# Kernel tuning notes

Measured on AMD Instinct MI355X. Metric: run time of the kernel, lower is better.

## Reference

```python
import jax, jax.numpy as jnp
import numpy as np

N, E, B = 10000, 160000, 256
IN, DESC = 57, 1217
# (in_dim, heads, out_per_head) for the 4 GATConv layers
CONV_DIMS = [(57, 5, 114), (570, 5, 171), (855, 5, 114), (570, 1, 570)]
FC_DIMS = [(1024 + DESC, 1024), (1024, 2048), (2048, 1024), (1024, 256), (256, 1)]


def setup_inputs() -> dict:
    key = jax.random.key(0)
    cnt = [0]
    def p(shape, scale=0.05):
        cnt[0] += 1
        return jax.random.normal(jax.random.fold_in(key, cnt[0]), shape, jnp.float32) * scale
    d = {}
    d["x"] = jax.random.normal(jax.random.fold_in(key, 100), (N, IN), jnp.float32)
    d["edge_index"] = jax.random.randint(jax.random.fold_in(key, 101), (2, E), 0, N)
    d["batch"] = jnp.sort(jax.random.randint(jax.random.fold_in(key, 102), (N,), 0, B))
    d["desc"] = jax.random.normal(jax.random.fold_in(key, 103), (B, DESC), jnp.float32)
    for i, (ci, H, C) in enumerate(CONV_DIMS, 1):
        d[f"W{i}"] = p((ci, H * C))
        d[f"as{i}"] = p((H, C))
        d[f"ad{i}"] = p((H, C))
        d[f"b{i}"] = jnp.zeros((H * C,), jnp.float32)
    d["Wg"] = p((570, 1024)); d["bg"] = jnp.zeros((1024,), jnp.float32)
    for i, (ci, co) in enumerate(FC_DIMS, 1):
        d[f"Wf{i}"] = p((ci, co))
        d[f"bf{i}"] = jnp.zeros((co,), jnp.float32)
    return d


def gat_conv(x, src, dst, W, a_src, a_dst, b):
    """PyG GATConv (eval mode: attention dropout off), self-loops already in src/dst."""
    n = x.shape[0]
    H, C = a_src.shape
    h = (x @ W).reshape(n, H, C)                      # [N,H,C]
    al_s = (h * a_src).sum(-1)                         # [N,H]
    al_d = (h * a_dst).sum(-1)                         # [N,H]
    e = jax.nn.leaky_relu(al_s[src] + al_d[dst], 0.2)  # [E,H]
    # segment softmax over destination node
    m = jax.ops.segment_max(e, dst, num_segments=n)
    e = jnp.exp(e - m[dst])
    s = jax.ops.segment_sum(e, dst, num_segments=n)
    alpha = e / (s[dst] + 1e-16)                       # [E,H]
    msg = h[src] * alpha[:, :, None]                   # [E,H,C]
    out = jax.ops.segment_sum(msg, dst, num_segments=n)
    return out.reshape(n, H * C) + b


def reference(x, edge_index, batch, desc,
              W1, as1, ad1, b1, W2, as2, ad2, b2,
              W3, as3, ad3, b3, W4, as4, ad4, b4,
              Wg, bg, Wf1, bf1, Wf2, bf2, Wf3, bf3, Wf4, bf4, Wf5, bf5):
    n = x.shape[0]
    loops = jnp.arange(n)
    src = jnp.concatenate([edge_index[0], loops])
    dst = jnp.concatenate([edge_index[1], loops])
    h = x
    for W, a_s, a_d, b in [(W1, as1, ad1, b1), (W2, as2, ad2, b2),
                           (W3, as3, ad3, b3), (W4, as4, ad4, b4)]:
        h = jax.nn.relu(gat_conv(h, src, dst, W, a_s, a_d, b))
    pooled = jax.ops.segment_sum(h, batch, num_segments=B)   # global_add_pool [B,570]
    g = pooled @ Wg + bg
    z = jnp.concatenate([g, desc], axis=1)                    # [B, 2241]
    z = jax.nn.relu(z @ Wf1 + bf1)
    z = jax.nn.relu(z @ Wf2 + bf2)
    z = jax.nn.relu(z @ Wf3 + bf3)
    z = jax.nn.relu(z @ Wf4 + bf4)
    return z @ Wf5 + bf5                                      # [B,1]
```

## Files before the change

kernel.cpp:

```cpp
#include <hip/hip_runtime.h>
#include <hip/hip_bf16.h>
#include <math.h>

#define NNODES 10000
#define NEDGES 160000
#define NB     256
#define ETOT   (NEDGES + NNODES)
#define INDIM  57
#define DESCD  1217

static inline size_t align256(size_t x) { return (x + 255) & ~size_t(255); }

typedef _Float16 half8_t __attribute__((ext_vector_type(8)));
typedef _Float16 half4v_t __attribute__((ext_vector_type(4)));
typedef _Float16 half2_t __attribute__((ext_vector_type(2)));
typedef float f32x4 __attribute__((ext_vector_type(4)));

__device__ inline void gload_lds16(const void* g, void* l) {
  __builtin_amdgcn_global_load_lds((const __attribute__((address_space(1))) void*)g,
                                   (__attribute__((address_space(3))) void*)l, 16, 0, 0);
}

__device__ inline float wave_sum(float v) {
#pragma unroll
  for (int o = 32; o > 0; o >>= 1) v += __shfl_xor(v, o);
  return v;
}

__global__ void count_kernel(const int* __restrict__ ei, int* __restrict__ deg) {
  int e = blockIdx.x * blockDim.x + threadIdx.x;
  if (e < ETOT) {
    int dst = (e < NEDGES) ? ei[NEDGES + e] : (e - NEDGES);
    atomicAdd(&deg[dst], 1);
  }
}

__global__ __launch_bounds__(1024) void scan_kernel(const int* __restrict__ deg,
                                                    int* __restrict__ row_ptr,
                                                    int* __restrict__ cursor) {
  __shared__ int part[1024];
  const int CHUNK = (NNODES + 1023) / 1024;
  int t = threadIdx.x;
  int start = t * CHUNK;
  int sum = 0;
  for (int i = 0; i < CHUNK; ++i) {
    int idx = start + i;
    if (idx < NNODES) sum += deg[idx];
  }
  part[t] = sum;
  __syncthreads();
  for (int off = 1; off < 1024; off <<= 1) {
    int v = (t >= off) ? part[t - off] : 0;
    __syncthreads();
    part[t] += v;
    __syncthreads();
  }
  int run = (t > 0) ? part[t - 1] : 0;
  for (int i = 0; i < CHUNK; ++i) {
    int idx = start + i;
    if (idx < NNODES) {
      row_ptr[idx] = run;
      cursor[idx] = run;
      run += deg[idx];
    }
  }
  if (t == 1023) row_ptr[NNODES] = ETOT;
}

__global__ void scatter_kernel(const int* __restrict__ ei, int* __restrict__ cursor,
                               int* __restrict__ csr_src) {
  int e = blockIdx.x * blockDim.x + threadIdx.x;
  if (e < ETOT) {
    int src, dst;
    if (e < NEDGES) { src = ei[e]; dst = ei[NEDGES + e]; }
    else            { src = e - NEDGES; dst = src; }
    int idx = atomicAdd(&cursor[dst], 1);
    csr_src[idx] = src;
  }
}

__global__ void convert_x_kernel(const float* __restrict__ x, _Float16* __restrict__ x16) {
  int t = blockIdx.x * blockDim.x + threadIdx.x;
  if (t >= NNODES * 64) return;
  int n = t >> 6, k = t & 63;
  x16[t] = (_Float16)((k < INDIM) ? x[n * INDIM + k] : 0.f);
}

struct TMat { const float* src; _Float16* dst; int K, N, Kpad, tiles_k, tile_base;
              int Cn, Cnp, Ck, Ckp; };
struct TParams { TMat m[9]; };

__global__ __launch_bounds__(256) void transpose_w_kernel(TParams P, int nm) {
  __shared__ float tile[64][65];
  int bt = blockIdx.x;
  int mi = 0;
#pragma unroll
  for (int i = 1; i < 9; ++i)
    if (i < nm && bt >= P.m[i].tile_base) mi = i;
  TMat m = P.m[mi];
  int lt = bt - m.tile_base;
  int tk = lt % m.tiles_k, tn = lt / m.tiles_k;
  int k0 = tk * 64, n0 = tn * 64;
  int c = threadIdx.x & 63, r4 = threadIdx.x >> 6;
#pragma unroll
  for (int i = 0; i < 16; ++i) {
    int kr = r4 + i * 4;
    int gk = k0 + kr, gn = n0 + c;
    tile[kr][c] = (gk < m.K && gn < m.N) ? m.src[(size_t)gk * m.N + gn] : 0.f;
  }
  __syncthreads();
#pragma unroll
  for (int i = 0; i < 16; ++i) {
    int nr = r4 + i * 4;
    int gn = n0 + nr, gk = k0 + c;
    if (gn < m.N && gk < m.K) {
      int np = gn + (gn / m.Cn) * (m.Cnp - m.Cn);
      int kp = gk + (gk / m.Ck) * (m.Ckp - m.Ck);
      m.dst[(size_t)np * m.Kpad + kp] = (_Float16)tile[c][nr];
    }
  }
}

struct LMat { const float* W; const float* as; const float* ad; _Float16* dst;
              int K, HC, C, H, Kpad, la, wave_base, Ck, Ckp; };

__global__ __launch_bounds__(256) void logitw_kernel(LMat m0, LMat m1, LMat m2, LMat m3,
                                                     int nwaves) {
  int gw = (blockIdx.x * 256 + threadIdx.x) >> 6;
  int lane = threadIdx.x & 63;
  if (gw >= nwaves) return;
  LMat m = m3;
  if (gw < m1.wave_base) m = m0;
  else if (gw < m2.wave_base) m = m1;
  else if (gw < m3.wave_base) m = m2;
  int li = gw - m.wave_base;
  int H2 = 2 * m.H;
  int k = li / H2, r = li - k * H2;
  int h = (r >= m.H) ? r - m.H : r;
  const float* a = (r >= m.H) ? m.ad : m.as;
  float s = 0.f;
  for (int c = lane; c < m.C; c += 64)
    s += m.W[(size_t)k * m.HC + h * m.C + c] * a[h * m.C + c];
  s = wave_sum(s);
  int kp = k + (k / m.Ck) * (m.Ckp - m.Ck);
  if (lane == 0) m.dst[(size_t)(m.la + r) * m.Kpad + kp] = (_Float16)s;
}

__global__ void pooled16_kernel(const float* __restrict__ pooled, _Float16* __restrict__ p16) {
  int t = blockIdx.x * blockDim.x + threadIdx.x;
  if (t >= NB * 576) return;
  int b = t / 576, c = t - b * 576;
  p16[t] = (_Float16)((c < 570) ? pooled[b * 570 + c] : 0.f);
}

__global__ void desc_fill_kernel(const float* __restrict__ desc, _Float16* __restrict__ z16) {
  int t = blockIdx.x * blockDim.x + threadIdx.x;
  if (t >= NB * 1280) return;
  int b = t / 1280, i = t - b * 1280;
  z16[(size_t)b * 2304 + 1024 + i] = (_Float16)((i < DESCD) ? desc[b * DESCD + i] : 0.f);
}

__global__ __launch_bounds__(256) void mfma_gemm_kernel(
    const _Float16* __restrict__ A, const _Float16* __restrict__ Bt,
    _Float16* __restrict__ C, int M, int Kpad, int Nreal, int ldc) {
  __shared__ __align__(16) char smem[32768];
  char* AsB = smem;
  char* BsB = smem + 16384;
  int tid = threadIdx.x;
  int lane = tid & 63, wid = tid >> 6;
  int l15 = lane & 15, g = lane >> 4;
  int wr = wid >> 1, wc = wid & 1;
  int m0 = blockIdx.y * 128, n0 = blockIdx.x * 128;
  f32x4 acc[4][4];
#pragma unroll
  for (int i = 0; i < 4; ++i)
#pragma unroll
    for (int j = 0; j < 4; ++j) acc[i][j] = (f32x4){0.f, 0.f, 0.f, 0.f};

  int KT = Kpad >> 6;
  int ra = tid >> 3;
  int c8 = tid & 7;
  const _Float16* srcA[4];
  const _Float16* srcB[4];
#pragma unroll
  for (int i = 0; i < 4; ++i) {
    int rr = i * 32 + ra;
    int cs = c8 ^ (rr & 7);
    int gaA = min(m0 + rr, M - 1);
    srcA[i] = A + (size_t)gaA * Kpad + cs * 8;
    srcB[i] = Bt + (size_t)(n0 + rr) * Kpad + cs * 8;
  }
  char* ldsA = AsB + wid * 1024;
  char* ldsB = BsB + wid * 1024;

  for (int kt = 0; kt < KT; ++kt) {
    int k0 = kt << 6;
    __syncthreads();
#pragma unroll
    for (int i = 0; i < 4; ++i) {
      gload_lds16(srcA[i] + k0, ldsA + i * 4096);
      gload_lds16(srcB[i] + k0, ldsB + i * 4096);
    }
    __syncthreads();
#pragma unroll
    for (int kk = 0; kk < 2; ++kk) {
      half8_t af[4], bf[4];
#pragma unroll
      for (int f = 0; f < 4; ++f) {
        int raf = wr * 64 + f * 16 + l15;
        af[f] = *(const half8_t*)(AsB + raf * 128 + (((kk * 4 + g) ^ (raf & 7)) << 4));
        int cb = wc * 64 + f * 16 + l15;
        bf[f] = *(const half8_t*)(BsB + cb * 128 + (((kk * 4 + g) ^ (cb & 7)) << 4));
      }
#pragma unroll
      for (int fm = 0; fm < 4; ++fm)
#pragma unroll
        for (int fn = 0; fn < 4; ++fn)
          acc[fm][fn] = __builtin_amdgcn_mfma_f32_16x16x32_f16(af[fm], bf[fn], acc[fm][fn], 0, 0, 0);
    }
  }
#pragma unroll
  for (int fm = 0; fm < 4; ++fm) {
    int gmb = m0 + wr * 64 + fm * 16 + g * 4;
#pragma unroll
    for (int fn = 0; fn < 4; ++fn) {
      int gn = n0 + wc * 64 + fn * 16 + l15;
      if (gn >= Nreal) continue;
#pragma unroll
      for (int j = 0; j < 4; ++j) {
        int gm = gmb + j;
        if (gm < M) C[(size_t)gm * ldc + gn] = (_Float16)acc[fm][fn][j];
      }
    }
  }
}

__global__ __launch_bounds__(256) void mfma_gemm64_kernel(
    const _Float16* __restrict__ A, const _Float16* __restrict__ Bt,
    const float* __restrict__ bias, _Float16* __restrict__ O,
    int Kpad, int ldc, int relu) {
  __shared__ __align__(16) char smem[16384];
  char* AsB = smem;
  char* BsB = smem + 8192;
  int tid = threadIdx.x;
  int lane = tid & 63, wid = tid >> 6;
  int l15 = lane & 15, g = lane >> 4;
  int wr = wid >> 1, wc = wid & 1;
  int m0 = blockIdx.y * 64, n0 = blockIdx.x * 64;
  f32x4 acc[2][2];
#pragma unroll
  for (int i = 0; i < 2; ++i)
#pragma unroll
    for (int j = 0; j < 2; ++j) acc[i][j] = (f32x4){0.f, 0.f, 0.f, 0.f};

  int KT = Kpad >> 6;
  int r = tid >> 2;
  half8_t pa[2], pb[2];
#pragma unroll
  for (int i = 0; i < 2; ++i) {
    int cc = (tid & 3) + 4 * i;
    int cs = cc ^ (r & 7);
    pa[i] = *(const half8_t*)(A + (size_t)(m0 + r) * Kpad + cs * 8);
    pb[i] = *(const half8_t*)(Bt + (size_t)(n0 + r) * Kpad + cs * 8);
  }
  for (int kt = 0; kt < KT; ++kt) {
    __syncthreads();
#pragma unroll
    for (int i = 0; i < 2; ++i) {
      int cc = (tid & 3) + 4 * i;
      *(half8_t*)(AsB + r * 128 + cc * 16) = pa[i];
      *(half8_t*)(BsB + r * 128 + cc * 16) = pb[i];
    }
    __syncthreads();
    if (kt + 1 < KT) {
      int k0 = (kt + 1) << 6;
#pragma unroll
      for (int i = 0; i < 2; ++i) {
        int cc = (tid & 3) + 4 * i;
        int cs = cc ^ (r & 7);
        pa[i] = *(const half8_t*)(A + (size_t)(m0 + r) * Kpad + k0 + cs * 8);
        pb[i] = *(const half8_t*)(Bt + (size_t)(n0 + r) * Kpad + k0 + cs * 8);
      }
    }
#pragma unroll
    for (int kk = 0; kk < 2; ++kk) {
      half8_t af[2], bf[2];
#pragma unroll
      for (int f = 0; f < 2; ++f) {
        int ra = wr * 32 + f * 16 + l15;
        af[f] = *(const half8_t*)(AsB + ra * 128 + (((kk * 4 + g) ^ (ra & 7)) << 4));
        int cb = wc * 32 + f * 16 + l15;
        bf[f] = *(const half8_t*)(BsB + cb * 128 + (((kk * 4 + g) ^ (cb & 7)) << 4));
      }
#pragma unroll
      for (int fm = 0; fm < 2; ++fm)
#pragma unroll
        for (int fn = 0; fn < 2; ++fn)
          acc[fm][fn] = __builtin_amdgcn_mfma_f32_16x16x32_f16(af[fm], bf[fn], acc[fm][fn], 0, 0, 0);
    }
  }
#pragma unroll
  for (int fm = 0; fm < 2; ++fm) {
    int gmb = m0 + wr * 32 + fm * 16 + g * 4;
#pragma unroll
    for (int fn = 0; fn < 2; ++fn) {
      int gn = n0 + wc * 32 + fn * 16 + l15;
      float bv = bias[gn];
#pragma unroll
      for (int j = 0; j < 4; ++j) {
        float v = acc[fm][fn][j] + bv;
        if (relu) v = fmaxf(v, 0.f);
        O[(size_t)(gmb + j) * ldc + gn] = (_Float16)v;
      }
    }
  }
}

__global__ __launch_bounds__(256) void fc5_kernel(const _Float16* __restrict__ A,
                                                  const float* __restrict__ w,
                                                  const float* __restrict__ b,
                                                  float* __restrict__ out) {
  int wid = threadIdx.x >> 6, lane = threadIdx.x & 63;
  int m = blockIdx.x * 4 + wid;
  if (m >= NB) return;
  float s = 0.f;
  for (int k = lane; k < 256; k += 64) s += (float)A[m * 256 + k] * w[k];
  s = wave_sum(s);
  if (lane == 0) out[m] = s + b[0];
}

template <int H>
__global__ __launch_bounds__(256) void att_kernel_t(const _Float16* __restrict__ hbuf,
                                                    int ldh, int la,
                                                    const int* __restrict__ row_ptr,
                                                    const int* __restrict__ csr_src,
                                                    _Float16* __restrict__ alpha_t,
                                                    float* __restrict__ sinv) {
  int wid = threadIdx.x >> 6, lane = threadIdx.x & 63;
  int n = blockIdx.x * 4 + wid;
  if (n >= NNODES) return;
  int rp = row_ptr[n], deg = row_ptr[n + 1] - rp;
  float ad[H], ssum[H];
#pragma unroll
  for (int h = 0; h < H; ++h) {
    ad[h] = (float)hbuf[(size_t)n * ldh + la + H + h];
    ssum[h] = 0.f;
  }
  for (int j = lane; j < deg; j += 64) {
    int s = csr_src[rp + j];
    half8_t v = *(const half8_t*)(hbuf + (size_t)s * ldh + la);
#pragma unroll
    for (int h = 0; h < H; ++h) {
      float e = (float)v[h] + ad[h];
      e = (e >= 0.f) ? e : 0.2f * e;
      e = fminf(e, 10.f);
      float x = expf(e);
      ssum[h] += x;
      alpha_t[(size_t)h * ETOT + rp + j] = (_Float16)x;
    }
  }
#pragma unroll
  for (int h = 0; h < H; ++h) {
    float s = wave_sum(ssum[h]);
    if (lane == 0) sinv[h * NNODES + n] = 1.f / (s + 1e-16f);
  }
}

__global__ __launch_bounds__(256) void agg_kernel(const _Float16* __restrict__ hbuf,
                                                  const _Float16* __restrict__ alpha_t,
                                                  const int* __restrict__ row_ptr,
                                                  const int* __restrict__ csr_src,
                                                  const float* __restrict__ bias,
                                                  const float* __restrict__ sinv,
                                                  _Float16* __restrict__ h16o,
                                                  int C, int Cpad, int ldh, int ldo,
                                                  int HCpad, int nchunks) {
  int wid = threadIdx.x >> 6, lane = threadIdx.x & 63;
  int gw = blockIdx.x * 4 + wid;
  int n = gw / nchunks, chunk = gw - n * nchunks;
  if (n >= NNODES) return;
  int k0 = chunk * 512 + lane * 8;
  if (k0 >= ldo) return;
  _Float16* op = h16o + (size_t)n * ldo + k0;
  if (k0 >= HCpad) { *(half8_t*)op = (half8_t){}; return; }
  int h0 = k0 / Cpad;
  int off = k0 - h0 * Cpad;
  const _Float16* A0 = alpha_t + (size_t)h0 * ETOT;
  const _Float16* hb = hbuf + k0;
  int rp = row_ptr[n], re = row_ptr[n + 1];
  half2_t acc0{}, acc1{}, acc2{}, acc3{};
  auto step = [&](int s, _Float16 a) {
    half8_t v = *(const half8_t*)(hb + (size_t)s * ldh);
    half2_t av{a, a};
    acc0 += av * half2_t{v[0], v[1]};
    acc1 += av * half2_t{v[2], v[3]};
    acc2 += av * half2_t{v[4], v[5]};
    acc3 += av * half2_t{v[6], v[7]};
  };
  int j = rp;
  for (; j < re && (j & 3); ++j) step(csr_src[j], A0[j]);
  for (; j + 8 <= re; j += 8) {
    int4 sa = *(const int4*)(csr_src + j);
    int4 sb = *(const int4*)(csr_src + j + 4);
    half4v_t aa = *(const half4v_t*)(A0 + j);
    half4v_t ab = *(const half4v_t*)(A0 + j + 4);
    step(sa.x, aa[0]); step(sa.y, aa[1]); step(sa.z, aa[2]); step(sa.w, aa[3]);
    step(sb.x, ab[0]); step(sb.y, ab[1]); step(sb.z, ab[2]); step(sb.w, ab[3]);
  }
  for (; j + 4 <= re; j += 4) {
    int4 sa = *(const int4*)(csr_src + j);
    half4v_t aa = *(const half4v_t*)(A0 + j);
    step(sa.x, aa[0]); step(sa.y, aa[1]); step(sa.z, aa[2]); step(sa.w, aa[3]);
  }
  for (; j < re; ++j) step(csr_src[j], A0[j]);
  float sc = sinv[h0 * NNODES + n];
  int base = h0 * C + off;
  int nreal = C - off;
  float af[8] = {(float)acc0[0], (float)acc0[1], (float)acc1[0], (float)acc1[1],
                 (float)acc2[0], (float)acc2[1], (float)acc3[0], (float)acc3[1]};
  half8_t o;
#pragma unroll
  for (int i = 0; i < 8; ++i) {
    float bv = bias[base + ((i < nreal) ? i : 0)];
    o[i] = (i < nreal) ? (_Float16)fmaxf(af[i] * sc + bv, 0.f) : (_Float16)0.f;
  }
  *(half8_t*)op = o;
}

__global__ __launch_bounds__(256) void pool_kernel(const _Float16* __restrict__ h4,
                                                   const int* __restrict__ batch,
                                                   float* __restrict__ pooled, int F, int ldh) {
  int wid = threadIdx.x >> 6, lane = threadIdx.x & 63;
  int n = blockIdx.x * 4 + wid;
  if (n >= NNODES) return;
  int b = batch[n];
  for (int k = lane; k < F; k += 64)
    atomicAdd(&pooled[(size_t)b * F + k], (float)h4[(size_t)n * ldh + k]);
}

extern "C" void kernel_launch(void* const* d_in, const int* in_sizes, int n_in,
                              void* d_out, int out_size, void* d_ws, size_t ws_size,
                              hipStream_t stream) {
  const float* x    = (const float*)d_in[0];
  const int*   ei   = (const int*)d_in[1];
  const int*   batch= (const int*)d_in[2];
  const float* desc = (const float*)d_in[3];
  const float* W1 = (const float*)d_in[4];  const float* as1 = (const float*)d_in[5];
  const float* ad1 = (const float*)d_in[6]; const float* b1 = (const float*)d_in[7];
  const float* W2 = (const float*)d_in[8];  const float* as2 = (const float*)d_in[9];
  const float* ad2 = (const float*)d_in[10];const float* b2 = (const float*)d_in[11];
  const float* W3 = (const float*)d_in[12]; const float* as3 = (const float*)d_in[13];
  const float* ad3 = (const float*)d_in[14];const float* b3 = (const float*)d_in[15];
  const float* W4 = (const float*)d_in[16]; const float* as4 = (const float*)d_in[17];
  const float* ad4 = (const float*)d_in[18];const float* b4 = (const float*)d_in[19];
  const float* Wg = (const float*)d_in[20]; const float* bg = (const float*)d_in[21];
  const float* Wf1 = (const float*)d_in[22];const float* bf1 = (const float*)d_in[23];
  const float* Wf2 = (const float*)d_in[24];const float* bf2 = (const float*)d_in[25];
  const float* Wf3 = (const float*)d_in[26];const float* bf3 = (const float*)d_in[27];
  const float* Wf4 = (const float*)d_in[28];const float* bf4 = (const float*)d_in[29];
  const float* Wf5 = (const float*)d_in[30];const float* bf5 = (const float*)d_in[31];
  float* out = (float*)d_out;

  char* p = (char*)d_ws;
  size_t off = 0;
  auto alloc = [&](size_t bytes) -> char* {
    char* r = p + off;
    off = align256(off + bytes);
    return r;
  };
  int*      deg     = (int*)alloc(sizeof(int) * NNODES);
  int*      row_ptr = (int*)alloc(sizeof(int) * (NNODES + 1));
  int*      cursor  = (int*)alloc(sizeof(int) * NNODES);
  int*      csr_src = (int*)alloc(sizeof(int) * ETOT);
  _Float16* alpha_t = (_Float16*)alloc(sizeof(_Float16) * (size_t)5 * ETOT);
  float*    sinv    = (float*)alloc(sizeof(float) * 5 * NNODES);
  _Float16* x16     = (_Float16*)alloc(sizeof(_Float16) * (size_t)NNODES * 64);
  _Float16* hA16    = (_Float16*)alloc(sizeof(_Float16) * ((size_t)NNODES * 896 + 1024));
  _Float16* h16     = (_Float16*)alloc(sizeof(_Float16) * ((size_t)NNODES * 896 + 1024));
  size_t wt_begin = off;
  _Float16* WtL1 = (_Float16*)alloc(sizeof(_Float16) * 640 * 64);
  _Float16* WtL2 = (_Float16*)alloc(sizeof(_Float16) * 896 * 640);
  _Float16* WtL3 = (_Float16*)alloc(sizeof(_Float16) * 640 * 896);
  _Float16* WtL4 = (_Float16*)alloc(sizeof(_Float16) * 640 * 640);
  _Float16* WtG  = (_Float16*)alloc(sizeof(_Float16) * 1024 * 576);
  _Float16* WtF1 = (_Float16*)alloc(sizeof(_Float16) * 1024 * 2304);
  _Float16* WtF2 = (_Float16*)alloc(sizeof(_Float16) * 2048 * 1024);
  _Float16* WtF3 = (_Float16*)alloc(sizeof(_Float16) * 1024 * 2048);
  _Float16* WtF4 = (_Float16*)alloc(sizeof(_Float16) * 256 * 1024);
  size_t wt_end = off;
  float*    pooled  = (float*)alloc(sizeof(float) * NB * 570);
  _Float16* p16     = (_Float16*)alloc(sizeof(_Float16) * NB * 576);
  _Float16* z16     = (_Float16*)alloc(sizeof(_Float16) * NB * 2304);
  _Float16* t16     = (_Float16*)alloc(sizeof(_Float16) * NB * 2048);
  _Float16* u16     = (_Float16*)alloc(sizeof(_Float16) * NB * 2048);
  _Float16* v16     = (_Float16*)alloc(sizeof(_Float16) * NB * 256);
  (void)ws_size;

  hipMemsetAsync(deg, 0, sizeof(int) * NNODES, stream);
  {
    dim3 g((ETOT + 255) / 256);
    count_kernel<<<g, 256, 0, stream>>>(ei, deg);
    scan_kernel<<<1, 1024, 0, stream>>>(deg, row_ptr, cursor);
    scatter_kernel<<<g, 256, 0, stream>>>(ei, cursor, csr_src);
  }
  convert_x_kernel<<<(NNODES * 64 + 255) / 256, 256, 0, stream>>>(x, x16);

  hipMemsetAsync(p + wt_begin, 0, wt_end - wt_begin, stream);
  {
    auto tiles = [](int K, int N) { return ((K + 63) / 64) * ((N + 63) / 64); };
    TParams tp;
    int base = 0;
    auto add = [&](int i, const float* src, _Float16* dst, int K, int N, int Kpad,
                   int Cn, int Cnp, int Ck, int Ckp) {
      tp.m[i] = { src, dst, K, N, Kpad, (K + 63) / 64, base, Cn, Cnp, Ck, Ckp };
      base += tiles(K, N);
    };
    add(0, W1,  WtL1, INDIM,        570,   64, 114, 120, INDIM, INDIM);
    add(1, W2,  WtL2, 570,          855,  640, 171, 176, 114, 120);
    add(2, W3,  WtL3, 855,          570,  896, 114, 120, 171, 176);
    add(3, W4,  WtL4, 570,          570,  640, 570, 570, 114, 120);
    add(4, Wg,  WtG,  570,          1024,  576, 1024, 1024, 570, 570);
    add(5, Wf1, WtF1, 1024 + DESCD, 1024, 2304, 1024, 1024, 2304, 2304);
    add(6, Wf2, WtF2, 1024,         2048, 1024, 2048, 2048, 1024, 1024);
    add(7, Wf3, WtF3, 2048,         1024, 2048, 1024, 1024, 2048, 2048);
    add(8, Wf4, WtF4, 1024,          256, 1024, 256, 256, 1024, 1024);
    transpose_w_kernel<<<base, 256, 0, stream>>>(tp, 9);
  }
  {
    LMat m0 = { W1, as1, ad1, WtL1, INDIM, 570, 114, 5,  64, 600, 0, INDIM, INDIM };
    LMat m1 = { W2, as2, ad2, WtL2, 570,   855, 171, 5, 640, 880, INDIM * 10, 114, 120 };
    LMat m2 = { W3, as3, ad3, WtL3, 855,   570, 114, 5, 896, 600, INDIM * 10 + 5700, 171, 176 };
    LMat m3 = { W4, as4, ad4, WtL4, 570,   570, 570, 1, 640, 576, INDIM * 10 + 5700 + 8550, 114, 120 };
    int nwaves = INDIM * 10 + 5700 + 8550 + 1140;
    logitw_kernel<<<(nwaves * 64 + 255) / 256, 256, 0, stream>>>(m0, m1, m2, m3, nwaves);
  }

  dim3 gnode((NNODES + 3) / 4);

  struct LayerDef { _Float16* Wt; const float* b;
                    int H, C, Cpad, HCpad, Kpad, Npad, ldh, la, Nreal, ldo; };
  LayerDef L[4] = {
    { WtL1, b1, 5, 114, 120, 600,  64, 640, 616, 600, 610, 640 },
    { WtL2, b2, 5, 171, 176, 880, 640, 896, 896, 880, 890, 896 },
    { WtL3, b3, 5, 114, 120, 600, 896, 640, 616, 600, 610, 640 },
    { WtL4, b4, 1, 570, 576, 576, 640, 640, 584, 576, 578, 576 },
  };
  for (int l = 0; l < 4; ++l) {
    {
      const _Float16* Ain = (l == 0) ? x16 : h16;
      dim3 g(L[l].Npad / 128, (NNODES + 127) / 128);
      mfma_gemm_kernel<<<g, 256, 0, stream>>>(Ain, L[l].Wt, hA16, NNODES, L[l].Kpad,
                                              L[l].Nreal, L[l].ldh);
    }
    if (L[l].H == 5)
      att_kernel_t<5><<<gnode, 256, 0, stream>>>(hA16, L[l].ldh, L[l].la,
                                                 row_ptr, csr_src, alpha_t, sinv);
    else
      att_kernel_t<1><<<gnode, 256, 0, stream>>>(hA16, L[l].ldh, L[l].la,
                                                 row_ptr, csr_src, alpha_t, sinv);
    {
      int nchunks = (L[l].ldo + 511) / 512;
      dim3 g((NNODES * nchunks + 3) / 4);
      agg_kernel<<<g, 256, 0, stream>>>(hA16, alpha_t, row_ptr, csr_src, L[l].b, sinv, h16,
                                        L[l].C, L[l].Cpad, L[l].ldh, L[l].ldo,
                                        L[l].HCpad, nchunks);
    }
  }

  hipMemsetAsync(pooled, 0, sizeof(float) * NB * 570, stream);
  pool_kernel<<<gnode, 256, 0, stream>>>(h16, batch, pooled, 570, 576);

  auto head_gemm = [&](const _Float16* A, const _Float16* Wt, const float* bias,
                       _Float16* O, int Kpad, int N, int ldc, int relu) {
    dim3 g(N / 64, NB / 64);
    mfma_gemm64_kernel<<<g, 256, 0, stream>>>(A, Wt, bias, O, Kpad, ldc, relu);
  };

  pooled16_kernel<<<(NB * 576 + 255) / 256, 256, 0, stream>>>(pooled, p16);
  head_gemm(p16, WtG, bg, z16, 576, 1024, 2304, 0);
  desc_fill_kernel<<<(NB * 1280 + 255) / 256, 256, 0, stream>>>(desc, z16);
  head_gemm(z16, WtF1, bf1, t16, 2304, 1024, 1024, 1);
  head_gemm(t16, WtF2, bf2, u16, 1024, 2048, 2048, 1);
  head_gemm(u16, WtF3, bf3, t16, 2048, 1024, 1024, 1);
  head_gemm(t16, WtF4, bf4, v16, 1024,  256,  256, 1);
  fc5_kernel<<<(NB + 3) / 4, 256, 0, stream>>>(v16, Wf5, bf5, out);
}
```

Before: 454.0 us.

## Use 64x64 GEMM for GAT layers and fuse aggregation chunks per wave

The dedicated 128x128 GEMM for the node-feature transforms is removed, and the 64x64 head GEMM (now with an optional bias) is reused over row-padded buffers, so the tail-row clamping goes away and the grid gets more blocks. The aggregation kernel now has one wave handle both 512-column chunks of a node. This removes the duplicated CSR index and alpha loads that happened when each chunk ran on its own wave. The GEMM output stride changes from the narrower ldh to Npad, which adds write traffic and padding columns, and the smaller tile lowers data reuse.

```diff
diff --git a/kernel.cpp b/kernel.cpp
--- a/kernel.cpp
+++ b/kernel.cpp
@@ -3,6 +3,7 @@
 #include <math.h>
 
 #define NNODES 10000
+#define NROWS  10048
 #define NEDGES 160000
 #define NB     256
 #define ETOT   (NEDGES + NNODES)
@@ -15,11 +16,6 @@
 typedef _Float16 half4v_t __attribute__((ext_vector_type(4)));
 typedef _Float16 half2_t __attribute__((ext_vector_type(2)));
 typedef float f32x4 __attribute__((ext_vector_type(4)));
-
-__device__ inline void gload_lds16(const void* g, void* l) {
-  __builtin_amdgcn_global_load_lds((const __attribute__((address_space(1))) void*)g,
-                                   (__attribute__((address_space(3))) void*)l, 16, 0, 0);
-}
 
 __device__ inline float wave_sum(float v) {
 #pragma unroll
@@ -160,81 +156,6 @@
   z16[(size_t)b * 2304 + 1024 + i] = (_Float16)((i < DESCD) ? desc[b * DESCD + i] : 0.f);
 }
 
-__global__ __launch_bounds__(256) void mfma_gemm_kernel(
-    const _Float16* __restrict__ A, const _Float16* __restrict__ Bt,
-    _Float16* __restrict__ C, int M, int Kpad, int Nreal, int ldc) {
-  __shared__ __align__(16) char smem[32768];
-  char* AsB = smem;
-  char* BsB = smem + 16384;
-  int tid = threadIdx.x;
-  int lane = tid & 63, wid = tid >> 6;
-  int l15 = lane & 15, g = lane >> 4;
-  int wr = wid >> 1, wc = wid & 1;
-  int m0 = blockIdx.y * 128, n0 = blockIdx.x * 128;
-  f32x4 acc[4][4];
-#pragma unroll
-  for (int i = 0; i < 4; ++i)
-#pragma unroll
-    for (int j = 0; j < 4; ++j) acc[i][j] = (f32x4){0.f, 0.f, 0.f, 0.f};
-
-  int KT = Kpad >> 6;
-  int ra = tid >> 3;
-  int c8 = tid & 7;
-  const _Float16* srcA[4];
-  const _Float16* srcB[4];
-#pragma unroll
-  for (int i = 0; i < 4; ++i) {
-    int rr = i * 32 + ra;
-    int cs = c8 ^ (rr & 7);
-    int gaA = min(m0 + rr, M - 1);
-    srcA[i] = A + (size_t)gaA * Kpad + cs * 8;
-    srcB[i] = Bt + (size_t)(n0 + rr) * Kpad + cs * 8;
-  }
-  char* ldsA = AsB + wid * 1024;
-  char* ldsB = BsB + wid * 1024;
-
-  for (int kt = 0; kt < KT; ++kt) {
-    int k0 = kt << 6;
-    __syncthreads();
-#pragma unroll
-    for (int i = 0; i < 4; ++i) {
-      gload_lds16(srcA[i] + k0, ldsA + i * 4096);
-      gload_lds16(srcB[i] + k0, ldsB + i * 4096);
-    }
-    __syncthreads();
-#pragma unroll
-    for (int kk = 0; kk < 2; ++kk) {
-      half8_t af[4], bf[4];
-#pragma unroll
-      for (int f = 0; f < 4; ++f) {
-        int raf = wr * 64 + f * 16 + l15;
-        af[f] = *(const half8_t*)(AsB + raf * 128 + (((kk * 4 + g) ^ (raf & 7)) << 4));
-        int cb = wc * 64 + f * 16 + l15;
-        bf[f] = *(const half8_t*)(BsB + cb * 128 + (((kk * 4 + g) ^ (cb & 7)) << 4));
-      }
-#pragma unroll
-      for (int fm = 0; fm < 4; ++fm)
-#pragma unroll
-        for (int fn = 0; fn < 4; ++fn)
-          acc[fm][fn] = __builtin_amdgcn_mfma_f32_16x16x32_f16(af[fm], bf[fn], acc[fm][fn], 0, 0, 0);
-    }
-  }
-#pragma unroll
-  for (int fm = 0; fm < 4; ++fm) {
-    int gmb = m0 + wr * 64 + fm * 16 + g * 4;
-#pragma unroll
-    for (int fn = 0; fn < 4; ++fn) {
-      int gn = n0 + wc * 64 + fn * 16 + l15;
-      if (gn >= Nreal) continue;
-#pragma unroll
-      for (int j = 0; j < 4; ++j) {
-        int gm = gmb + j;
-        if (gm < M) C[(size_t)gm * ldc + gn] = (_Float16)acc[fm][fn][j];
-      }
-    }
-  }
-}
-
 __global__ __launch_bounds__(256) void mfma_gemm64_kernel(
     const _Float16* __restrict__ A, const _Float16* __restrict__ Bt,
     const float* __restrict__ bias, _Float16* __restrict__ O,
@@ -305,7 +226,7 @@
 #pragma unroll
     for (int fn = 0; fn < 2; ++fn) {
       int gn = n0 + wc * 32 + fn * 16 + l15;
-      float bv = bias[gn];
+      float bv = bias ? bias[gn] : 0.f;
 #pragma unroll
       for (int j = 0; j < 4; ++j) {
         float v = acc[fm][fn][j] + bv;
@@ -374,57 +295,80 @@
                                                   const float* __restrict__ sinv,
                                                   _Float16* __restrict__ h16o,
                                                   int C, int Cpad, int ldh, int ldo,
-                                                  int HCpad, int nchunks) {
+                                                  int HCpad) {
   int wid = threadIdx.x >> 6, lane = threadIdx.x & 63;
-  int gw = blockIdx.x * 4 + wid;
-  int n = gw / nchunks, chunk = gw - n * nchunks;
+  int n = blockIdx.x * 4 + wid;
   if (n >= NNODES) return;
-  int k0 = chunk * 512 + lane * 8;
-  if (k0 >= ldo) return;
-  _Float16* op = h16o + (size_t)n * ldo + k0;
-  if (k0 >= HCpad) { *(half8_t*)op = (half8_t){}; return; }
-  int h0 = k0 / Cpad;
-  int off = k0 - h0 * Cpad;
-  const _Float16* A0 = alpha_t + (size_t)h0 * ETOT;
-  const _Float16* hb = hbuf + k0;
+  int k0a = lane * 8;
+  int k0b = 512 + lane * 8;
+  bool actB = (k0b < HCpad);
+  int h0a = k0a / Cpad, offa = k0a - h0a * Cpad;
+  int h0b = actB ? (k0b / Cpad) : 0;
+  int offb = k0b - h0b * Cpad;
+  const _Float16* A0a = alpha_t + (size_t)h0a * ETOT;
+  const _Float16* A0b = alpha_t + (size_t)h0b * ETOT;
+  const _Float16* hba = hbuf + k0a;
+  const _Float16* hbb = hbuf + (actB ? k0b : k0a);
   int rp = row_ptr[n], re = row_ptr[n + 1];
-  half2_t acc0{}, acc1{}, acc2{}, acc3{};
-  auto step = [&](int s, _Float16 a) {
-    half8_t v = *(const half8_t*)(hb + (size_t)s * ldh);
-    half2_t av{a, a};
-    acc0 += av * half2_t{v[0], v[1]};
-    acc1 += av * half2_t{v[2], v[3]};
-    acc2 += av * half2_t{v[4], v[5]};
-    acc3 += av * half2_t{v[6], v[7]};
+  half2_t a0{}, a1{}, a2{}, a3{}, b0{}, b1{}, b2{}, b3{};
+  auto step = [&](int s, _Float16 aa, _Float16 ab) {
+    half8_t va = *(const half8_t*)(hba + (size_t)s * ldh);
+    half2_t av{aa, aa};
+    a0 += av * half2_t{va[0], va[1]};
+    a1 += av * half2_t{va[2], va[3]};
+    a2 += av * half2_t{va[4], va[5]};
+    a3 += av * half2_t{va[6], va[7]};
+    if (actB) {
+      half8_t vb = *(const half8_t*)(hbb + (size_t)s * ldh);
+      half2_t bv{ab, ab};
+      b0 += bv * half2_t{vb[0], vb[1]};
+      b1 += bv * half2_t{vb[2], vb[3]};
+      b2 += bv * half2_t{vb[4], vb[5]};
+      b3 += bv * half2_t{vb[6], vb[7]};
+    }
   };
   int j = rp;
-  for (; j < re && (j & 3); ++j) step(csr_src[j], A0[j]);
-  for (; j + 8 <= re; j += 8) {
-    int4 sa = *(const int4*)(csr_src + j);
-    int4 sb = *(const int4*)(csr_src + j + 4);
-    half4v_t aa = *(const half4v_t*)(A0 + j);
-    half4v_t ab = *(const half4v_t*)(A0 + j + 4);
-    step(sa.x, aa[0]); step(sa.y, aa[1]); step(sa.z, aa[2]); step(sa.w, aa[3]);
-    step(sb.x, ab[0]); step(sb.y, ab[1]); step(sb.z, ab[2]); step(sb.w, ab[3]);
-  }
+  for (; j < re && (j & 3); ++j) step(csr_src[j], A0a[j], A0b[j]);
   for (; j + 4 <= re; j += 4) {
-    int4 sa = *(const int4*)(csr_src + j);
-    half4v_t aa = *(const half4v_t*)(A0 + j);
-    step(sa.x, aa[0]); step(sa.y, aa[1]); step(sa.z, aa[2]); step(sa.w, aa[3]);
-  }
-  for (; j < re; ++j) step(csr_src[j], A0[j]);
-  float sc = sinv[h0 * NNODES + n];
-  int base = h0 * C + off;
-  int nreal = C - off;
-  float af[8] = {(float)acc0[0], (float)acc0[1], (float)acc1[0], (float)acc1[1],
-                 (float)acc2[0], (float)acc2[1], (float)acc3[0], (float)acc3[1]};
-  half8_t o;
-#pragma unroll
-  for (int i = 0; i < 8; ++i) {
-    float bv = bias[base + ((i < nreal) ? i : 0)];
-    o[i] = (i < nreal) ? (_Float16)fmaxf(af[i] * sc + bv, 0.f) : (_Float16)0.f;
-  }
-  *(half8_t*)op = o;
+    int4 s4 = *(const int4*)(csr_src + j);
+    half4v_t aav = *(const half4v_t*)(A0a + j);
+    half4v_t abv = *(const half4v_t*)(A0b + j);
+    step(s4.x, aav[0], abv[0]);
+    step(s4.y, aav[1], abv[1]);
+    step(s4.z, aav[2], abv[2]);
+    step(s4.w, aav[3], abv[3]);
+  }
+  for (; j < re; ++j) step(csr_src[j], A0a[j], A0b[j]);
+  {
+    float sc = sinv[h0a * NNODES + n];
+    int base = h0a * C + offa;
+    int nreal = C - offa;
+    float af[8] = {(float)a0[0], (float)a0[1], (float)a1[0], (float)a1[1],
+                   (float)a2[0], (float)a2[1], (float)a3[0], (float)a3[1]};
+    half8_t o;
+#pragma unroll
+    for (int i = 0; i < 8; ++i) {
+      float bv = (i < nreal) ? bias[base + i] : 0.f;
+      o[i] = (i < nreal) ? (_Float16)fmaxf(af[i] * sc + bv, 0.f) : (_Float16)0.f;
+    }
+    *(half8_t*)(h16o + (size_t)n * ldo + k0a) = o;
+  }
+  if (k0b < ldo) {
+    half8_t o{};
+    if (actB) {
+      float sc = sinv[h0b * NNODES + n];
+      int base = h0b * C + offb;
+      int nreal = C - offb;
+      float bf8[8] = {(float)b0[0], (float)b0[1], (float)b1[0], (float)b1[1],
+                      (float)b2[0], (float)b2[1], (float)b3[0], (float)b3[1]};
+#pragma unroll
+      for (int i = 0; i < 8; ++i) {
+        float bv = (i < nreal) ? bias[base + i] : 0.f;
+        o[i] = (i < nreal) ? (_Float16)fmaxf(bf8[i] * sc + bv, 0.f) : (_Float16)0.f;
+      }
+    }
+    *(half8_t*)(h16o + (size_t)n * ldo + k0b) = o;
+  }
 }
 
 __global__ __launch_bounds__(256) void pool_kernel(const _Float16* __restrict__ h4,
@@ -474,9 +418,9 @@
   int*      csr_src = (int*)alloc(sizeof(int) * ETOT);
   _Float16* alpha_t = (_Float16*)alloc(sizeof(_Float16) * (size_t)5 * ETOT);
   float*    sinv    = (float*)alloc(sizeof(float) * 5 * NNODES);
-  _Float16* x16     = (_Float16*)alloc(sizeof(_Float16) * (size_t)NNODES * 64);
-  _Float16* hA16    = (_Float16*)alloc(sizeof(_Float16) * ((size_t)NNODES * 896 + 1024));
-  _Float16* h16     = (_Float16*)alloc(sizeof(_Float16) * ((size_t)NNODES * 896 + 1024));
+  _Float16* x16     = (_Float16*)alloc(sizeof(_Float16) * (size_t)NROWS * 64);
+  _Float16* hA16    = (_Float16*)alloc(sizeof(_Float16) * (size_t)NROWS * 896);
+  _Float16* h16     = (_Float16*)alloc(sizeof(_Float16) * (size_t)NROWS * 896);
   size_t wt_begin = off;
   _Float16* WtL1 = (_Float16*)alloc(sizeof(_Float16) * 640 * 64);
   _Float16* WtL2 = (_Float16*)alloc(sizeof(_Float16) * 896 * 640);
@@ -538,33 +482,29 @@
   dim3 gnode((NNODES + 3) / 4);
 
   struct LayerDef { _Float16* Wt; const float* b;
-                    int H, C, Cpad, HCpad, Kpad, Npad, ldh, la, Nreal, ldo; };
+                    int H, C, Cpad, HCpad, Kpad, Npad, la, ldo; };
   LayerDef L[4] = {
-    { WtL1, b1, 5, 114, 120, 600,  64, 640, 616, 600, 610, 640 },
-    { WtL2, b2, 5, 171, 176, 880, 640, 896, 896, 880, 890, 896 },
-    { WtL3, b3, 5, 114, 120, 600, 896, 640, 616, 600, 610, 640 },
-    { WtL4, b4, 1, 570, 576, 576, 640, 640, 584, 576, 578, 576 },
+    { WtL1, b1, 5, 114, 120, 600,  64, 640, 600, 640 },
+    { WtL2, b2, 5, 171, 176, 880, 640, 896, 880, 896 },
+    { WtL3, b3, 5, 114, 120, 600, 896, 640, 600, 640 },
+    { WtL4, b4, 1, 570, 576, 576, 640, 640, 576, 576 },
   };
   for (int l = 0; l < 4; ++l) {
     {
       const _Float16* Ain = (l == 0) ? x16 : h16;
-      dim3 g(L[l].Npad / 128, (NNODES + 127) / 128);
-      mfma_gemm_kernel<<<g, 256, 0, stream>>>(Ain, L[l].Wt, hA16, NNODES, L[l].Kpad,
-                                              L[l].Nreal, L[l].ldh);
+      dim3 g(L[l].Npad / 64, NROWS / 64);
+      mfma_gemm64_kernel<<<g, 256, 0, stream>>>(Ain, L[l].Wt, nullptr, hA16,
+                                                L[l].Kpad, L[l].Npad, 0);
     }
     if (L[l].H == 5)
-      att_kernel_t<5><<<gnode, 256, 0, stream>>>(hA16, L[l].ldh, L[l].la,
+      att_kernel_t<5><<<gnode, 256, 0, stream>>>(hA16, L[l].Npad, L[l].la,
                                                  row_ptr, csr_src, alpha_t, sinv);
     else
-      att_kernel_t<1><<<gnode, 256, 0, stream>>>(hA16, L[l].ldh, L[l].la,
+      att_kernel_t<1><<<gnode, 256, 0, stream>>>(hA16, L[l].Npad, L[l].la,
                                                  row_ptr, csr_src, alpha_t, sinv);
-    {
-      int nchunks = (L[l].ldo + 511) / 512;
-      dim3 g((NNODES * nchunks + 3) / 4);
-      agg_kernel<<<g, 256, 0, stream>>>(hA16, alpha_t, row_ptr, csr_src, L[l].b, sinv, h16,
-                                        L[l].C, L[l].Cpad, L[l].ldh, L[l].ldo,
-                                        L[l].HCpad, nchunks);
-    }
+    agg_kernel<<<gnode, 256, 0, stream>>>(hA16, alpha_t, row_ptr, csr_src, L[l].b, sinv, h16,
+                                          L[l].C, L[l].Cpad, L[l].Npad, L[l].ldo,
+                                          L[l].HCpad);
   }
 
   hipMemsetAsync(pooled, 0, sizeof(float) * NB * 570, stream);
```

Measured after the change: 485.8 us. 1.07x slower.
